# Kernel optimization log

Measured on AMD Instinct MI355X. Metric: run time of the kernel, lower is better.

The kernel has to match this reference:

```python
import jax, jax.numpy as jnp
import numpy as np

DIM = 1536      # model dim
NH = 12         # num heads
HD = 128        # head dim
F, H, W = 3, 26, 48   # video latent grid (frames, height, width)
S = F * H * W   # sequence length = 3744
B = 1
EPS = 1e-6
C2 = HD // 2    # 64 rotary pairs per head
SPLITS = [C2 - 2 * (C2 // 3), C2 // 3, C2 // 3]  # [22, 21, 21] for (f, h, w)


def _rope_angles():
    """Wan rope_params: concat of per-axis inverse-frequency angle tables, [1024, 64]."""
    def rp(dim):  # returns [1024, dim//2]
        inv = 1.0 / (10000.0 ** (np.arange(0, dim, 2, dtype=np.float64) / dim))
        return np.outer(np.arange(1024, dtype=np.float64), inv)
    a = np.concatenate([rp(HD - 4 * (HD // 6)), rp(2 * (HD // 6)), rp(2 * (HD // 6))], axis=1)
    return jnp.asarray(a, jnp.float32)


def setup_inputs() -> dict:
    key = jax.random.key(0)
    ks = jax.random.split(key, 9)
    std = DIM ** -0.5
    return {
        "x": jax.random.normal(ks[0], (B, S, DIM), jnp.float32),
        "wq": jax.random.normal(ks[1], (DIM, DIM), jnp.float32) * std,
        "bq": jnp.zeros((DIM,), jnp.float32),
        "wk": jax.random.normal(ks[2], (DIM, DIM), jnp.float32) * std,
        "bk": jnp.zeros((DIM,), jnp.float32),
        "wv": jax.random.normal(ks[3], (DIM, DIM), jnp.float32) * std,
        "bv": jnp.zeros((DIM,), jnp.float32),
        "wo": jax.random.normal(ks[4], (DIM, DIM), jnp.float32) * std,
        "bo": jnp.zeros((DIM,), jnp.float32),
        "gq": jnp.ones((DIM,), jnp.float32),   # WanRMSNorm weight for q
        "gk": jnp.ones((DIM,), jnp.float32),   # WanRMSNorm weight for k
        "freqs": _rope_angles(),                # [1024, 64] rotary angles
        "seq_lens": jnp.full((B,), S, jnp.int32),
    }


def _rmsnorm(y, g):
    return y * jax.lax.rsqrt(jnp.mean(jnp.square(y), axis=-1, keepdims=True) + EPS) * g


def _rope_grid(freqs):
    """Build per-position rotary angles [S, C2] from the 3D grid (F,H,W)."""
    af = freqs[:F, :SPLITS[0]]                       # [F, 22]
    ah = freqs[:H, SPLITS[0]:SPLITS[0] + SPLITS[1]]  # [H, 21]
    aw = freqs[:W, SPLITS[0] + SPLITS[1]:]           # [W, 21]
    ang = jnp.concatenate([
        jnp.broadcast_to(af[:, None, None, :], (F, H, W, SPLITS[0])),
        jnp.broadcast_to(ah[None, :, None, :], (F, H, W, SPLITS[1])),
        jnp.broadcast_to(aw[None, None, :, :], (F, H, W, SPLITS[2])),
    ], axis=-1)
    return ang.reshape(S, C2)


def _rope_apply(t, cos, sin):
    # t: [B, S, NH, HD]; pairs (even, odd) rotated by angle.
    tp = t.reshape(B, S, NH, C2, 2)
    xr, xi = tp[..., 0], tp[..., 1]
    yr = xr * cos - xi * sin
    yi = xr * sin + xi * cos
    return jnp.stack([yr, yi], axis=-1).reshape(B, S, NH, HD)


def reference(x, wq, bq, wk, bk, wv, bv, wo, bo, gq, gk, freqs, seq_lens):
    q = _rmsnorm(x @ wq.T + bq, gq).reshape(B, S, NH, HD)
    k = _rmsnorm(x @ wk.T + bk, gk).reshape(B, S, NH, HD)
    v = (x @ wv.T + bv).reshape(B, S, NH, HD)

    ang = _rope_grid(freqs)                    # [S, C2]
    cos = jnp.cos(ang)[None, :, None, :]       # [1, S, 1, C2]
    sin = jnp.sin(ang)[None, :, None, :]
    q = _rope_apply(q, cos, sin)
    k = _rope_apply(k, cos, sin)

    scale = HD ** -0.5
    scores = jnp.einsum('bqhd,bkhd->bhqk', q, k) * scale   # [B, NH, S, S]
    kmask = jnp.arange(S)[None, :] < seq_lens[:, None]     # [B, S]
    scores = jnp.where(kmask[:, None, None, :], scores, jnp.float32(-1e9))
    attn = jax.nn.softmax(scores, axis=-1)
    out = jnp.einsum('bhqk,bkhd->bqhd', attn, v).reshape(B, S, DIM)
    return out @ wo.T + bo
```

## Files before the change

kernel.cpp:

```cpp
#include <hip/hip_runtime.h>
#include <stdint.h>


#define DIM   1536
#define S_TOT 3744
#define NHEAD 12
#define HD    128
#define QT    59
#define KVT   59
#define KSPLIT 2

using short8 = __attribute__((ext_vector_type(8))) short;
using f32x4  = __attribute__((ext_vector_type(4))) float;
using f32x16 = __attribute__((ext_vector_type(16))) float;
using f32x2  = __attribute__((ext_vector_type(2))) float;

__device__ __forceinline__ unsigned short f2bf(float f) {
  unsigned u = __builtin_bit_cast(unsigned, f);
  u += 0x7fffu + ((u >> 16) & 1u);
  return (unsigned short)(u >> 16);
}

__device__ __forceinline__ short8 mk8(unsigned a, unsigned b, unsigned c, unsigned d) {
  union { unsigned u[4]; short8 s; } x;
  x.u[0] = a; x.u[1] = b; x.u[2] = c; x.u[3] = d;
  return x.s;
}

__device__ __forceinline__ void gl_lds16(const void* g, void* l) {
  auto gp = (const __attribute__((address_space(1))) unsigned int*)g;
  auto lp = (__attribute__((address_space(3))) unsigned int*)(uintptr_t)l;
  __builtin_amdgcn_global_load_lds(gp, lp, 16, 0, 0);
}

#define NX4 (S_TOT * DIM / 4)
#define NW4 (DIM * DIM / 4)
__global__ __launch_bounds__(256) void cvt5_kernel(
    const float* __restrict__ x, const float* __restrict__ wq,
    const float* __restrict__ wk, const float* __restrict__ wv,
    const float* __restrict__ wo,
    unsigned short* __restrict__ xb, unsigned short* __restrict__ wqb,
    unsigned short* __restrict__ wkb, unsigned short* __restrict__ wvb,
    unsigned short* __restrict__ wob) {
  int gid = blockIdx.x * 256 + threadIdx.x;
  const float* src; unsigned short* dst; int off;
  if (gid < NX4)                { src = x;  dst = xb;  off = gid; }
  else if (gid < NX4 + NW4)     { src = wq; dst = wqb; off = gid - NX4; }
  else if (gid < NX4 + 2 * NW4) { src = wk; dst = wkb; off = gid - NX4 - NW4; }
  else if (gid < NX4 + 3 * NW4) { src = wv; dst = wvb; off = gid - NX4 - 2 * NW4; }
  else if (gid < NX4 + 4 * NW4) { src = wo; dst = wob; off = gid - NX4 - 3 * NW4; }
  else return;
  float4 v = ((const float4*)src)[off];
  ushort4 o;
  o.x = f2bf(v.x); o.y = f2bf(v.y); o.z = f2bf(v.z); o.w = f2bf(v.w);
  ((ushort4*)dst)[off] = o;
}

__device__ __forceinline__ void gemm_body(const unsigned short* __restrict__ A,
                                          const unsigned short* __restrict__ W,
                                          const float* __restrict__ bias,
                                          float* __restrict__ outF,
                                          unsigned short* __restrict__ outB,
                                          int M, int mode) {
  constexpr int K = DIM, N = DIM;
  __shared__ unsigned short As[128 * 32];
  __shared__ unsigned short Ws[128 * 32];
  int tid = threadIdx.x;
  int w = tid >> 6, lane = tid & 63;
  int wr = w >> 1, wc = w & 1, q4 = lane >> 4, ql = lane & 15;
  int m0 = blockIdx.y * 128, n0 = blockIdx.x * 128;

  f32x4 acc[4][4];
  const f32x4 zero4 = {0.f, 0.f, 0.f, 0.f};
#pragma unroll
  for (int i = 0; i < 4; i++)
#pragma unroll
    for (int j = 0; j < 4; j++) acc[i][j] = zero4;

  for (int k0 = 0; k0 < K; k0 += 32) {
    __syncthreads();
#pragma unroll
    for (int r = 0; r < 2; r++) {
      int idx = r * 256 + tid;
      int row = idx >> 2, ch = idx & 3;
      int am = m0 + row; am = (am < M) ? am : (M - 1);
      gl_lds16(A + (size_t)am * K + k0 + ch * 8, &As[idx * 8]);
      gl_lds16(W + (size_t)(n0 + row) * K + k0 + ch * 8, &Ws[idx * 8]);
    }
    __syncthreads();
    short8 af[4], wf[4];
#pragma unroll
    for (int i = 0; i < 4; i++)
      af[i] = *(const short8*)&As[(wr * 64 + i * 16 + ql) * 32 + q4 * 8];
#pragma unroll
    for (int j = 0; j < 4; j++)
      wf[j] = *(const short8*)&Ws[(wc * 64 + j * 16 + ql) * 32 + q4 * 8];
#pragma unroll
    for (int i = 0; i < 4; i++)
#pragma unroll
      for (int j = 0; j < 4; j++)
        acc[i][j] = __builtin_amdgcn_mfma_f32_16x16x32_bf16(af[i], wf[j], acc[i][j], 0, 0, 0);
  }

  float bb[4];
#pragma unroll
  for (int j = 0; j < 4; j++) bb[j] = bias[n0 + wc * 64 + j * 16 + ql];
#pragma unroll
  for (int i = 0; i < 4; i++) {
#pragma unroll
    for (int rg = 0; rg < 4; rg++) {
      int row = m0 + wr * 64 + i * 16 + q4 * 4 + rg;
      if (row < M) {
#pragma unroll
        for (int j = 0; j < 4; j++) {
          int col = n0 + wc * 64 + j * 16 + ql;
          float v = acc[i][j][rg] + bb[j];
          if (mode == 0) outF[(size_t)row * N + col] = v;
          else           outB[(size_t)row * N + col] = f2bf(v);
        }
      }
    }
  }
}

__global__ __launch_bounds__(256) void gemm_qkv_kernel(
    const unsigned short* __restrict__ xb,
    const unsigned short* __restrict__ wqb, const unsigned short* __restrict__ wkb,
    const unsigned short* __restrict__ wvb,
    const float* __restrict__ bq, const float* __restrict__ bk, const float* __restrict__ bv,
    float* __restrict__ Yq, float* __restrict__ Yk, unsigned short* __restrict__ Vb) {
  int z = blockIdx.z;
  const unsigned short* W = (z == 0) ? wqb : ((z == 1) ? wkb : wvb);
  const float* bias       = (z == 0) ? bq  : ((z == 1) ? bk  : bv);
  float* outF             = (z == 0) ? Yq  : Yk;
  gemm_body(xb, W, bias, outF, Vb, S_TOT, (z == 2) ? 1 : 0);
}

__global__ __launch_bounds__(256) void gemm_out_kernel(
    const unsigned short* __restrict__ AO, const unsigned short* __restrict__ wob,
    const float* __restrict__ bo, float* __restrict__ out) {
  gemm_body(AO, wob, bo, out, nullptr, S_TOT, 0);
}

__global__ __launch_bounds__(256) void normrope_kernel(
    const float* __restrict__ Yq, const float* __restrict__ Yk,
    const float* __restrict__ gq, const float* __restrict__ gk,
    const float* __restrict__ freqs,
    unsigned short* __restrict__ Qb, unsigned short* __restrict__ Kb) {
  int s = blockIdx.x;
  int tid = threadIdx.x;
  int w = tid >> 6, lane = tid & 63;
  const f32x2* yq2 = (const f32x2*)(Yq + (size_t)s * DIM);
  const f32x2* yk2 = (const f32x2*)(Yk + (size_t)s * DIM);
  f32x2 vq[3], vk[3];
  float ssq = 0.f, ssk = 0.f;
#pragma unroll
  for (int r = 0; r < 3; r++) {
    int p = tid + 256 * r;
    vq[r] = yq2[p]; vk[r] = yk2[p];
    ssq += vq[r].x * vq[r].x + vq[r].y * vq[r].y;
    ssk += vk[r].x * vk[r].x + vk[r].y * vk[r].y;
  }
#pragma unroll
  for (int d = 1; d < 64; d <<= 1) {
    ssq += __shfl_xor(ssq, d);
    ssk += __shfl_xor(ssk, d);
  }
  __shared__ float rq[4], rk[4];
  if (lane == 0) { rq[w] = ssq; rk[w] = ssk; }
  __syncthreads();
  float tq = rq[0] + rq[1] + rq[2] + rq[3];
  float tk = rk[0] + rk[1] + rk[2] + rk[3];
  const float SM_L2 = 0.08838834764831845f * 1.4426950408889634f;
  float invq = rsqrtf(tq * (1.f / DIM) + 1e-6f) * SM_L2;
  float invk = rsqrtf(tk * (1.f / DIM) + 1e-6f);

  int fi = s / (26 * 48);
  int hi = (s / 48) % 26;
  int wi = s % 48;
#pragma unroll
  for (int r = 0; r < 3; r++) {
    int p = tid + 256 * r;
    int c = p & 63;
    int frow = (c < 22) ? fi : ((c < 43) ? hi : wi);
    float ang = freqs[frow * 64 + c];
    float sn, cs;
    __sincosf(ang, &sn, &cs);
    {
      float a = vq[r].x * invq * gq[2 * p];
      float b = vq[r].y * invq * gq[2 * p + 1];
      ushort2 o; o.x = f2bf(a * cs - b * sn); o.y = f2bf(a * sn + b * cs);
      ((ushort2*)Qb)[(size_t)s * (DIM / 2) + p] = o;
    }
    {
      float a = vk[r].x * invk * gk[2 * p];
      float b = vk[r].y * invk * gk[2 * p + 1];
      ushort2 o; o.x = f2bf(a * cs - b * sn); o.y = f2bf(a * sn + b * cs);
      ((ushort2*)Kb)[(size_t)s * (DIM / 2) + p] = o;
    }
  }
}

__global__ __launch_bounds__(256) void vtrans_kernel(const unsigned short* __restrict__ Vb,
                                                     unsigned short* __restrict__ Vt) {
  int d0 = blockIdx.x * 64, s0 = blockIdx.y * 64;
  __shared__ unsigned short t[64][65];
  int tid = threadIdx.x;
#pragma unroll
  for (int r = 0; r < 4; r++) {
    int idx = r * 256 + tid;
    int sr = idx >> 4, c4 = (idx & 15) * 4;
    ushort4 v; v.x = v.y = v.z = v.w = 0;
    int s = s0 + sr;
    if (s < S_TOT) v = *(const ushort4*)(Vb + (size_t)s * DIM + d0 + c4);
    t[sr][c4 + 0] = v.x; t[sr][c4 + 1] = v.y; t[sr][c4 + 2] = v.z; t[sr][c4 + 3] = v.w;
  }
  __syncthreads();
#pragma unroll
  for (int r = 0; r < 4; r++) {
    int idx = r * 256 + tid;
    int dr = idx >> 4, s4 = (idx & 15) * 4;
    if (s0 + s4 < S_TOT) {
      ushort4 v;
      v.x = t[s4 + 0][dr]; v.y = t[s4 + 1][dr]; v.z = t[s4 + 2][dr]; v.w = t[s4 + 3][dr];
      *(ushort4*)(Vt + (size_t)(d0 + dr) * S_TOT + s0 + s4) = v;
    }
  }
}

__global__ __launch_bounds__(128, 2) void attn_kernel(
    const unsigned short* __restrict__ Qb, const unsigned short* __restrict__ Kb,
    const unsigned short* __restrict__ Vt,
    float* __restrict__ Opart, float2* __restrict__ Ml,
    const int* __restrict__ seq_lens) {
  const int NWG = QT * NHEAD * KSPLIT;
  int bid = blockIdx.x;
  int xcd = bid & 7, bix = bid >> 3;
  const int qc = NWG >> 3;
  int wg = xcd * qc + bix;
  int qt  = wg % QT;
  int rem = wg / QT;
  int h    = rem >> 1;
  int sidx = rem & 1;
  int tbeg = sidx ? 30 : 0;
  int tend = sidx ? KVT : 30;

  int tid = threadIdx.x;
  int wv = tid >> 6, lane = tid & 63;
  int lo = lane & 31, hf = lane >> 5;
  int seqlen = seq_lens[0]; if (seqlen > S_TOT) seqlen = S_TOT;

  __shared__ unsigned short Kl[64 * 128];
  __shared__ unsigned short Vl[128 * 64];

  int q0 = qt * 64 + wv * 32;
  bool wact = (q0 < S_TOT);
  const size_t hoff = (size_t)h * HD;

  short8 qf[8];
  {
    int qrow = q0 + lo; if (qrow > S_TOT - 1) qrow = S_TOT - 1;
#pragma unroll
    for (int ks = 0; ks < 8; ks++)
      qf[ks] = *(const short8*)(Qb + (size_t)qrow * DIM + hoff + ks * 16 + hf * 8);
  }

  f32x16 o[4];
#pragma unroll
  for (int dq = 0; dq < 4; dq++)
#pragma unroll
    for (int r = 0; r < 16; r++) o[dq][r] = 0.f;
  float m_run = -3.0e38f, l_run = 0.f;

  for (int t = tbeg; t < tend; ++t) {
    int k0 = t * 64;
    __syncthreads();
    {
      const unsigned short* kseg = Kb + (size_t)k0 * DIM + hoff;
#pragma unroll
      for (int r = 0; r < 8; r++) {
        int idx = r * 128 + tid;
        int row = idx >> 4, c = idx & 15;
        int g = c ^ (row & 15);
        gl_lds16(kseg + (size_t)row * DIM + g * 8, &Kl[idx * 8]);
      }
      int kmax = S_TOT - 8 - k0;
#pragma unroll
      for (int r = 0; r < 8; r++) {
        int idx = r * 128 + tid;
        int row = idx >> 3, c = idx & 7;
        int g = c ^ (row & 7);
        int kc = g * 8; if (kc > kmax) kc = kmax;
        gl_lds16(Vt + (hoff + row) * S_TOT + k0 + kc, &Vl[idx * 8]);
      }
    }
    __syncthreads();
    if (!wact) continue;

    f32x16 s0, s1;
#pragma unroll
    for (int r = 0; r < 16; r++) { s0[r] = 0.f; s1[r] = 0.f; }
    __builtin_amdgcn_s_setprio(1);
#pragma unroll
    for (int ks = 0; ks < 8; ks++) {
      int sl = ((ks * 2 + hf) ^ (lo & 15)) * 8;
      short8 kf0 = *(const short8*)&Kl[lo * 128 + sl];
      short8 kf1 = *(const short8*)&Kl[(32 + lo) * 128 + sl];
      s0 = __builtin_amdgcn_mfma_f32_32x32x16_bf16(kf0, qf[ks], s0, 0, 0, 0);
      s1 = __builtin_amdgcn_mfma_f32_32x32x16_bf16(kf1, qf[ks], s1, 0, 0, 0);
    }
    __builtin_amdgcn_s_setprio(0);

    if (k0 + 64 > seqlen) {
#pragma unroll
      for (int r = 0; r < 16; r++) {
        int key0 = k0 + (r & 3) + 8 * (r >> 2) + 4 * hf;
        if (key0      >= seqlen) s0[r] = -3.0e38f;
        if (key0 + 32 >= seqlen) s1[r] = -3.0e38f;
      }
    }

    float mloc = s0[0];
#pragma unroll
    for (int r = 1; r < 16; r++) mloc = fmaxf(mloc, s0[r]);
#pragma unroll
    for (int r = 0; r < 16; r++) mloc = fmaxf(mloc, s1[r]);
    mloc = fmaxf(mloc, __shfl_xor(mloc, 32));

    if (!__all(mloc <= m_run + 8.0f)) {
      float mnew = fmaxf(m_run, mloc);
      float alpha = exp2f(m_run - mnew);
      m_run = mnew;
      l_run *= alpha;
      int lb = lane & 32;
      float ar[16];
#pragma unroll
      for (int r = 0; r < 16; r++)
        ar[r] = __shfl(alpha, ((r & 3) + 8 * (r >> 2) + 4 * hf) | lb);
#pragma unroll
      for (int dq = 0; dq < 4; dq++)
#pragma unroll
        for (int r = 0; r < 16; r++) o[dq][r] *= ar[r];
    }

    float lloc = 0.f;
    short8 pa[4];
    {
      float p[16];
#pragma unroll
      for (int r = 0; r < 16; r++) { p[r] = exp2f(s0[r] - m_run); lloc += p[r]; }
      unsigned pr[8];
#pragma unroll
      for (int i = 0; i < 8; i++)
        asm("v_cvt_pk_bf16_f32 %0, %1, %2" : "=v"(pr[i]) : "v"(p[2 * i]), "v"(p[2 * i + 1]));
      asm volatile("v_permlane32_swap_b32 %0, %1" : "+v"(pr[0]), "+v"(pr[2]));
      asm volatile("v_permlane32_swap_b32 %0, %1" : "+v"(pr[1]), "+v"(pr[3]));
      asm volatile("v_permlane32_swap_b32 %0, %1" : "+v"(pr[4]), "+v"(pr[6]));
      asm volatile("v_permlane32_swap_b32 %0, %1" : "+v"(pr[5]), "+v"(pr[7]));
      pa[0] = mk8(pr[0], pr[1], pr[2], pr[3]);
      pa[1] = mk8(pr[4], pr[5], pr[6], pr[7]);
    }
    {
      float p[16];
#pragma unroll
      for (int r = 0; r < 16; r++) { p[r] = exp2f(s1[r] - m_run); lloc += p[r]; }
      unsigned pr[8];
#pragma unroll
      for (int i = 0; i < 8; i++)
        asm("v_cvt_pk_bf16_f32 %0, %1, %2" : "=v"(pr[i]) : "v"(p[2 * i]), "v"(p[2 * i + 1]));
      asm volatile("v_permlane32_swap_b32 %0, %1" : "+v"(pr[0]), "+v"(pr[2]));
      asm volatile("v_permlane32_swap_b32 %0, %1" : "+v"(pr[1]), "+v"(pr[3]));
      asm volatile("v_permlane32_swap_b32 %0, %1" : "+v"(pr[4]), "+v"(pr[6]));
      asm volatile("v_permlane32_swap_b32 %0, %1" : "+v"(pr[5]), "+v"(pr[7]));
      pa[2] = mk8(pr[0], pr[1], pr[2], pr[3]);
      pa[3] = mk8(pr[4], pr[5], pr[6], pr[7]);
    }
    lloc += __shfl_xor(lloc, 32);
    l_run += lloc;

    __builtin_amdgcn_s_setprio(1);
#pragma unroll
    for (int kh2 = 0; kh2 < 4; kh2++) {
      int sl = ((kh2 * 2 + hf) ^ (lo & 7)) * 8;
#pragma unroll
      for (int dq = 0; dq < 4; dq++) {
        short8 vb = *(const short8*)&Vl[(dq * 32 + lo) * 64 + sl];
        o[dq] = __builtin_amdgcn_mfma_f32_32x32x16_bf16(pa[kh2], vb, o[dq], 0, 0, 0);
      }
    }
    __builtin_amdgcn_s_setprio(0);
  }

  if (wact) {
    size_t ob = (((size_t)sidx * NHEAD + h) * QT + qt) * (64 * 128);
#pragma unroll
    for (int dq = 0; dq < 4; dq++)
#pragma unroll
      for (int r = 0; r < 16; r++) {
        int row = wv * 32 + (r & 3) + 8 * (r >> 2) + 4 * hf;
        Opart[ob + (size_t)row * 128 + dq * 32 + lo] = o[dq][r];
      }
    if (lane < 32) {
      float2 ml; ml.x = m_run; ml.y = l_run;
      Ml[((size_t)(sidx * NHEAD + h) * QT + qt) * 64 + wv * 32 + lo] = ml;
    }
  }
}

__global__ __launch_bounds__(256) void reduce_kernel(
    const float* __restrict__ Opart, const float2* __restrict__ Ml,
    unsigned short* __restrict__ AO) {
  int flat = blockIdx.x * 256 + threadIdx.x;
  int d = flat & 127;
  int r = flat >> 7;
  int h = r / S_TOT;
  int q = r - h * S_TOT;
  int qt = q >> 6, qi = q & 63;
  size_t ob = (((size_t)h * QT) + qt) * (64 * 128) + (size_t)qi * 128 + d;
  const size_t so = (size_t)NHEAD * QT * 64 * 128;
  int mb = (h * QT + qt) * 64 + qi;
  const int sm = NHEAD * QT * 64;
  float2 ml0 = Ml[mb], ml1 = Ml[mb + sm];
  float mm = fmaxf(ml0.x, ml1.x);
  float w0 = exp2f(ml0.x - mm), w1 = exp2f(ml1.x - mm);
  float l = w0 * ml0.y + w1 * ml1.y;
  float v = (w0 * Opart[ob] + w1 * Opart[ob + so]) / l;
  AO[(size_t)q * DIM + h * HD + d] = f2bf(v);
}

extern "C" void kernel_launch(void* const* d_in, const int* in_sizes, int n_in,
                              void* d_out, int out_size, void* d_ws, size_t ws_size,
                              hipStream_t stream) {
  const float* x    = (const float*)d_in[0];
  const float* wq   = (const float*)d_in[1];
  const float* bq   = (const float*)d_in[2];
  const float* wk   = (const float*)d_in[3];
  const float* bk   = (const float*)d_in[4];
  const float* wv   = (const float*)d_in[5];
  const float* bv   = (const float*)d_in[6];
  const float* wo   = (const float*)d_in[7];
  const float* bo   = (const float*)d_in[8];
  const float* gq   = (const float*)d_in[9];
  const float* gk   = (const float*)d_in[10];
  const float* freqs = (const float*)d_in[11];
  const int*   seq  = (const int*)d_in[12];

  char* ws = (char*)d_ws;
  const size_t SZ_X = (size_t)S_TOT * DIM * 2;
  const size_t SZ_W = (size_t)DIM * DIM * 2;
  const size_t SZ_Y = (size_t)S_TOT * DIM * 4;

  size_t off = 0;
  unsigned short* xb  = (unsigned short*)(ws + off); off += SZ_X;
  unsigned short* wob = (unsigned short*)(ws + off); off += SZ_W;
  float*          Yq  = (float*)(ws + off);          off += SZ_Y;
  float*          Yk  = (float*)(ws + off);          off += SZ_Y;
  unsigned short* wqb = (unsigned short*)(ws + off); off += SZ_W;
  unsigned short* wkb = (unsigned short*)(ws + off); off += SZ_W;
  unsigned short* wvb = (unsigned short*)(ws + off); off += SZ_W;
  unsigned short* Vb  = (unsigned short*)(ws + off); off += SZ_X;
  unsigned short* Qb  = (unsigned short*)(ws + off); off += SZ_X;
  unsigned short* Kb  = (unsigned short*)(ws + off); off += SZ_X;
  unsigned short* Vt  = (unsigned short*)(ws + off); off += SZ_X;
  unsigned short* AO  = (unsigned short*)(ws + off); off += SZ_X;

  float*  Opart = (float*)Yq;
  float2* Ml    = (float2*)((char*)Yq +
                  (size_t)KSPLIT * NHEAD * QT * 64 * 128 * sizeof(float));

  int total4 = NX4 + 4 * NW4;
  cvt5_kernel<<<dim3((total4 + 255) / 256), 256, 0, stream>>>(
      x, wq, wk, wv, wo, xb, wqb, wkb, wvb, wob);

  gemm_qkv_kernel<<<dim3(DIM / 128, (S_TOT + 127) / 128, 3), 256, 0, stream>>>(
      xb, wqb, wkb, wvb, bq, bk, bv, Yq, Yk, Vb);

  normrope_kernel<<<dim3(S_TOT), 256, 0, stream>>>(Yq, Yk, gq, gk, freqs, Qb, Kb);

  vtrans_kernel<<<dim3(DIM / 64, (S_TOT + 63) / 64), 256, 0, stream>>>(Vb, Vt);

  attn_kernel<<<dim3(QT * NHEAD * KSPLIT), 128, 0, stream>>>(
      Qb, Kb, Vt, Opart, Ml, seq);

  reduce_kernel<<<dim3(NHEAD * S_TOT * HD / 256), 256, 0, stream>>>(Opart, Ml, AO);

  gemm_out_kernel<<<dim3(DIM / 128, (S_TOT + 127) / 128), 256, 0, stream>>>(
      AO, wob, bo, (float*)d_out);
}
```

Before: 451.4 us.

## Double-buffer K/V LDS staging and widen attention Q tile to four waves

The attention kernel now runs four waves per workgroup covering 128 query rows, halving the number of workgroups and sharing each K/V tile across twice as many queries. K/V tiles are staged into a double-buffered LDS array, and the next tile's async loads are issued before computing on the current one, with explicit vmcnt waits and barriers. The partial-output and reduce indexing are updated for the 128-row tiles. This doubles LDS use per workgroup and may reduce occupancy, and the larger partial buffer now spills into the freed Yk region.

Result: faster. 417.4 us (-7.5%).

```diff
diff --git a/kernel.cpp b/kernel.cpp
--- a/kernel.cpp
+++ b/kernel.cpp
@@ -6,7 +6,7 @@
 #define S_TOT 3744
 #define NHEAD 12
 #define HD    128
-#define QT    59
+#define QT2   30
 #define KVT   59
 #define KSPLIT 2
 
@@ -228,18 +228,18 @@
   }
 }
 
-__global__ __launch_bounds__(128, 2) void attn_kernel(
+__global__ __launch_bounds__(256, 2) void attn_kernel(
     const unsigned short* __restrict__ Qb, const unsigned short* __restrict__ Kb,
     const unsigned short* __restrict__ Vt,
     float* __restrict__ Opart, float2* __restrict__ Ml,
     const int* __restrict__ seq_lens) {
-  const int NWG = QT * NHEAD * KSPLIT;
+  const int NWG = QT2 * NHEAD * KSPLIT;
   int bid = blockIdx.x;
   int xcd = bid & 7, bix = bid >> 3;
   const int qc = NWG >> 3;
   int wg = xcd * qc + bix;
-  int qt  = wg % QT;
-  int rem = wg / QT;
+  int qt  = wg % QT2;
+  int rem = wg / QT2;
   int h    = rem >> 1;
   int sidx = rem & 1;
   int tbeg = sidx ? 30 : 0;
@@ -250,12 +250,33 @@
   int lo = lane & 31, hf = lane >> 5;
   int seqlen = seq_lens[0]; if (seqlen > S_TOT) seqlen = S_TOT;
 
-  __shared__ unsigned short Kl[64 * 128];
-  __shared__ unsigned short Vl[128 * 64];
-
-  int q0 = qt * 64 + wv * 32;
+  __shared__ unsigned short Kl[2][64 * 128];
+  __shared__ unsigned short Vl[2][128 * 64];
+
+  int q0 = qt * 128 + wv * 32;
   bool wact = (q0 < S_TOT);
   const size_t hoff = (size_t)h * HD;
+
+  auto stage = [&](int buf, int t) {
+    int k0 = t * 64;
+    const unsigned short* kseg = Kb + (size_t)k0 * DIM + hoff;
+#pragma unroll
+    for (int r = 0; r < 4; r++) {
+      int idx = r * 256 + tid;
+      int row = idx >> 4, c = idx & 15;
+      int g = c ^ (row & 15);
+      gl_lds16(kseg + (size_t)row * DIM + g * 8, &Kl[buf][idx * 8]);
+    }
+    int kmax = S_TOT - 8 - k0;
+#pragma unroll
+    for (int r = 0; r < 4; r++) {
+      int idx = r * 256 + tid;
+      int row = idx >> 3, c = idx & 7;
+      int g = c ^ (row & 7);
+      int kc = g * 8; if (kc > kmax) kc = kmax;
+      gl_lds16(Vt + (hoff + row) * S_TOT + k0 + kc, &Vl[buf][idx * 8]);
+    }
+  };
 
   short8 qf[8];
   {
@@ -264,6 +285,7 @@
     for (int ks = 0; ks < 8; ks++)
       qf[ks] = *(const short8*)(Qb + (size_t)qrow * DIM + hoff + ks * 16 + hf * 8);
   }
+  asm volatile("s_waitcnt vmcnt(0)" ::: "memory");
 
   f32x16 o[4];
 #pragma unroll
@@ -272,29 +294,22 @@
     for (int r = 0; r < 16; r++) o[dq][r] = 0.f;
   float m_run = -3.0e38f, l_run = 0.f;
 
+  stage(0, tbeg);
+
   for (int t = tbeg; t < tend; ++t) {
+    int cur = (t - tbeg) & 1;
     int k0 = t * 64;
-    __syncthreads();
-    {
-      const unsigned short* kseg = Kb + (size_t)k0 * DIM + hoff;
-#pragma unroll
-      for (int r = 0; r < 8; r++) {
-        int idx = r * 128 + tid;
-        int row = idx >> 4, c = idx & 15;
-        int g = c ^ (row & 15);
-        gl_lds16(kseg + (size_t)row * DIM + g * 8, &Kl[idx * 8]);
-      }
-      int kmax = S_TOT - 8 - k0;
-#pragma unroll
-      for (int r = 0; r < 8; r++) {
-        int idx = r * 128 + tid;
-        int row = idx >> 3, c = idx & 7;
-        int g = c ^ (row & 7);
-        int kc = g * 8; if (kc > kmax) kc = kmax;
-        gl_lds16(Vt + (hoff + row) * S_TOT + k0 + kc, &Vl[idx * 8]);
-      }
-    }
-    __syncthreads();
+    __builtin_amdgcn_s_barrier();
+    asm volatile("" ::: "memory");
+    if (t + 1 < tend) {
+      stage(cur ^ 1, t + 1);
+      asm volatile("s_waitcnt vmcnt(8)" ::: "memory");
+    } else {
+      asm volatile("s_waitcnt vmcnt(0)" ::: "memory");
+    }
+    __builtin_amdgcn_sched_barrier(0);
+    __builtin_amdgcn_s_barrier();
+    asm volatile("" ::: "memory");
     if (!wact) continue;
 
     f32x16 s0, s1;
@@ -304,8 +319,8 @@
 #pragma unroll
     for (int ks = 0; ks < 8; ks++) {
       int sl = ((ks * 2 + hf) ^ (lo & 15)) * 8;
-      short8 kf0 = *(const short8*)&Kl[lo * 128 + sl];
-      short8 kf1 = *(const short8*)&Kl[(32 + lo) * 128 + sl];
+      short8 kf0 = *(const short8*)&Kl[cur][lo * 128 + sl];
+      short8 kf1 = *(const short8*)&Kl[cur][(32 + lo) * 128 + sl];
       s0 = __builtin_amdgcn_mfma_f32_32x32x16_bf16(kf0, qf[ks], s0, 0, 0, 0);
       s1 = __builtin_amdgcn_mfma_f32_32x32x16_bf16(kf1, qf[ks], s1, 0, 0, 0);
     }
@@ -384,7 +399,7 @@
       int sl = ((kh2 * 2 + hf) ^ (lo & 7)) * 8;
 #pragma unroll
       for (int dq = 0; dq < 4; dq++) {
-        short8 vb = *(const short8*)&Vl[(dq * 32 + lo) * 64 + sl];
+        short8 vb = *(const short8*)&Vl[cur][(dq * 32 + lo) * 64 + sl];
         o[dq] = __builtin_amdgcn_mfma_f32_32x32x16_bf16(pa[kh2], vb, o[dq], 0, 0, 0);
       }
     }
@@ -392,7 +407,7 @@
   }
 
   if (wact) {
-    size_t ob = (((size_t)sidx * NHEAD + h) * QT + qt) * (64 * 128);
+    size_t ob = (((size_t)sidx * NHEAD + h) * QT2 + qt) * (128 * 128);
 #pragma unroll
     for (int dq = 0; dq < 4; dq++)
 #pragma unroll
@@ -402,7 +417,7 @@
       }
     if (lane < 32) {
       float2 ml; ml.x = m_run; ml.y = l_run;
-      Ml[((size_t)(sidx * NHEAD + h) * QT + qt) * 64 + wv * 32 + lo] = ml;
+      Ml[((size_t)(sidx * NHEAD + h) * QT2 + qt) * 128 + wv * 32 + lo] = ml;
     }
   }
 }
@@ -415,11 +430,11 @@
   int r = flat >> 7;
   int h = r / S_TOT;
   int q = r - h * S_TOT;
-  int qt = q >> 6, qi = q & 63;
-  size_t ob = (((size_t)h * QT) + qt) * (64 * 128) + (size_t)qi * 128 + d;
-  const size_t so = (size_t)NHEAD * QT * 64 * 128;
-  int mb = (h * QT + qt) * 64 + qi;
-  const int sm = NHEAD * QT * 64;
+  int qt = q >> 7, qi = q & 127;
+  size_t ob = (((size_t)h * QT2) + qt) * (128 * 128) + (size_t)qi * 128 + d;
+  const size_t so = (size_t)NHEAD * QT2 * 128 * 128;
+  int mb = (h * QT2 + qt) * 128 + qi;
+  const int sm = NHEAD * QT2 * 128;
   float2 ml0 = Ml[mb], ml1 = Ml[mb + sm];
   float mm = fmaxf(ml0.x, ml1.x);
   float w0 = exp2f(ml0.x - mm), w1 = exp2f(ml1.x - mm);
@@ -466,7 +481,7 @@
 
   float*  Opart = (float*)Yq;
   float2* Ml    = (float2*)((char*)Yq +
-                  (size_t)KSPLIT * NHEAD * QT * 64 * 128 * sizeof(float));
+                  (size_t)KSPLIT * NHEAD * QT2 * 128 * 128 * sizeof(float));
 
   int total4 = NX4 + 4 * NW4;
   cvt5_kernel<<<dim3((total4 + 255) / 256), 256, 0, stream>>>(
@@ -479,7 +494,7 @@
 
   vtrans_kernel<<<dim3(DIM / 64, (S_TOT + 63) / 64), 256, 0, stream>>>(Vb, Vt);
 
-  attn_kernel<<<dim3(QT * NHEAD * KSPLIT), 128, 0, stream>>>(
+  attn_kernel<<<dim3(QT2 * NHEAD * KSPLIT), 256, 0, stream>>>(
       Qb, Kb, Vt, Opart, Ml, seq);
 
   reduce_kernel<<<dim3(NHEAD * S_TOT * HD / 256), 256, 0, stream>>>(Opart, Ml, AO);
```
